# Kernel tuning notes

Measured on AMD Instinct MI355X. Metric: run time of the kernel, lower is better.

The kernel has to match this reference:

```python
import jax, jax.numpy as jnp
import numpy as np

D_MODEL = 1024
N_HEADS = 16
D_HEAD = D_MODEL // N_HEADS
LN_EPS = 1e-5


def setup_inputs() -> dict:
    key = jax.random.key(0)
    ks = jax.random.split(key, 8)
    B, T = 4, 2048
    s = 1.0 / np.sqrt(D_MODEL)
    return {
        "encoder_seq": jax.random.normal(ks[0], (B, T, D_MODEL), jnp.float32),
        "decoder_seq": jax.random.normal(ks[1], (B, T, D_MODEL), jnp.float32),
        "Wq": jax.random.normal(ks[2], (D_MODEL, D_MODEL), jnp.float32) * s,
        "bq": jnp.zeros((D_MODEL,), jnp.float32),
        "Wk": jax.random.normal(ks[3], (D_MODEL, D_MODEL), jnp.float32) * s,
        "bk": jnp.zeros((D_MODEL,), jnp.float32),
        "Wv": jax.random.normal(ks[4], (D_MODEL, D_MODEL), jnp.float32) * s,
        "bv": jnp.zeros((D_MODEL,), jnp.float32),
        "ln_gamma": jnp.ones((D_MODEL,), jnp.float32),
        "ln_beta": jnp.zeros((D_MODEL,), jnp.float32),
    }


def layer_norm(x, gamma, beta):
    mu = jnp.mean(x, axis=-1, keepdims=True)
    var = jnp.mean(jnp.square(x - mu), axis=-1, keepdims=True)
    return (x - mu) * jax.lax.rsqrt(var + LN_EPS) * gamma + beta


def reference(encoder_seq, decoder_seq, Wq, bq, Wk, bk, Wv, bv, ln_gamma, ln_beta):
    B, T_dec, _ = decoder_seq.shape
    T_enc = encoder_seq.shape[1]
    # projections (torch Linear: x @ W^T + b)
    q = (decoder_seq @ Wq.T + bq).reshape(B, T_dec, N_HEADS, D_HEAD)
    k = (encoder_seq @ Wk.T + bk).reshape(B, T_enc, N_HEADS, D_HEAD)
    v = (encoder_seq @ Wv.T + bv).reshape(B, T_enc, N_HEADS, D_HEAD)
    scale = 1.0 / np.sqrt(D_HEAD)
    # softmax-free attention: scale*(Q K^T) V == scale * Q (K^T V); avoid [T_dec,T_enc]
    kv = jnp.einsum("bthd,bthe->bhde", k, v)          # [B,H,dh,dh]
    att = jnp.einsum("bqhd,bhde->bqhe", q, kv) * scale  # [B,T_dec,H,dh]
    att = att.reshape(B, T_dec, D_MODEL)
    # dropout is identity in eval mode; residual + LayerNorm
    return layer_norm(att + decoder_seq, ln_gamma, ln_beta)
```

## Files before the change

### kernel.cpp

```cpp
#include <hip/hip_runtime.h>
#include <hip/hip_bf16.h>
#include <stdint.h>
#include <stddef.h>

typedef __attribute__((ext_vector_type(8))) __bf16 bf16x8;
typedef __attribute__((ext_vector_type(4))) float f32x4;

#define DMODEL 1024
#define HEADS  16
#define BATCH  4
#define TSEQ   2048
#define MROWS  (BATCH * TSEQ)
#define NE     (MROWS * DMODEL)
#define NW     (DMODEL * DMODEL)

#define MiB (size_t)1048576
#define QB_OFF   ((size_t)0)
#define KB_OFF   (16 * MiB)
#define VB_OFF   (32 * MiB)
#define ENC_OFF  (48 * MiB)
#define DEC_OFF  (64 * MiB)
#define KVP_OFF  (64 * MiB)
#define WB_OFF   (80 * MiB)
#define KVT_OFF  (86 * MiB)

__global__ __launch_bounds__(256)
void conv_all(const float* __restrict__ enc, const float* __restrict__ dec,
              const float* __restrict__ Wq, const float* __restrict__ Wk,
              const float* __restrict__ Wv,
              __bf16* __restrict__ encB, __bf16* __restrict__ decB,
              __bf16* __restrict__ WB)
{
    const int i = (blockIdx.x * 256 + threadIdx.x) * 8;
    const float* src;
    __bf16* dst;
    int off;
    if (i < NE)            { src = enc; dst = encB; off = i; }
    else if (i < 2 * NE)   { src = dec; dst = decB; off = i - NE; }
    else {
        const int j = i - 2 * NE;
        const int sel = j >> 20;
        off = j & (NW - 1);
        src = (sel == 0) ? Wq : (sel == 1) ? Wk : Wv;
        dst = WB + (size_t)sel * NW;
    }
    f32x4 a = *(const f32x4*)(src + off);
    f32x4 b = *(const f32x4*)(src + off + 4);
    bf16x8 o;
#pragma unroll
    for (int j = 0; j < 4; ++j) { o[j] = (__bf16)a[j]; o[j + 4] = (__bf16)b[j]; }
    *(bf16x8*)(dst + off) = o;
}

__device__ __forceinline__ int swz4(int row) { return (row & 3) ^ ((row >> 2) & 3); }

__device__ __forceinline__ bf16x8 frag32(const __bf16* reg, int rowl, int g4)
{
    const int slot = g4 ^ swz4(rowl);
    return *(const bf16x8*)(reg + rowl * 32 + slot * 8);
}

__device__ __forceinline__ void stage_half32(const __bf16* gbase, int kt,
                                             __bf16* reg, int tid)
{
    const int row = tid >> 2, slot = tid & 3;
    const __bf16* src = gbase + (size_t)row * DMODEL + kt * 32
                        + ((slot ^ swz4(row)) << 3);
    __builtin_amdgcn_global_load_lds(
        (const __attribute__((address_space(1))) void*)src,
        (__attribute__((address_space(3))) void*)(reg + tid * 8), 16, 0, 0);
}

#define VMW(N)  asm volatile("s_waitcnt vmcnt(" #N ")" ::: "memory")
#define LGKM0() asm volatile("s_waitcnt lgkmcnt(0)" ::: "memory")

__global__ __launch_bounds__(512, 4)
void qkv_gemm(const __bf16* __restrict__ decB, const __bf16* __restrict__ encB,
              const __bf16* __restrict__ WB,
              const float* __restrict__ bq, const float* __restrict__ bk,
              const float* __restrict__ bv,
              __bf16* __restrict__ Qb, __bf16* __restrict__ Kb,
              __bf16* __restrict__ Vb)
{
    __shared__ __align__(16) __bf16 ldsA[2 * 4096];
    __shared__ __align__(16) __bf16 ldsB[2 * 8192];

    const int tid  = threadIdx.x;
    const int lane = tid & 63;
    const int wv   = tid >> 6;
    const int wm   = wv >> 2;
    const int wn   = wv & 3;
    const int bh2  = wn >> 1;
    const int l4   = lane & 15;
    const int g4   = lane >> 4;

    const int bid  = blockIdx.x;
    const int slab = bid & 7;
    const int idx  = bid >> 3;
    const int r    = idx >> 3;
    const int sel  = r >> 2;
    const int bn   = r & 3;
    const int bm   = slab * 8 + (idx & 7);

    const __bf16* A    = (sel == 0) ? decB : encB;
    const __bf16* Wb   = WB + (size_t)sel * NW + (size_t)(bn * 256) * DMODEL;
    const float*  bias = (sel == 0) ? bq : (sel == 1) ? bk : bv;
    __bf16*       C    = (sel == 0) ? Qb : (sel == 1) ? Kb : Vb;

    const __bf16* Ab = A + (size_t)(bm * 128) * DMODEL;

    auto stage_tile = [&](int par, int kt) {
        stage_half32(Ab,                        kt, ldsA + par * 4096,        tid);
        stage_half32(Wb,                        kt, ldsB + par * 8192,        tid);
        stage_half32(Wb + (size_t)128 * DMODEL, kt, ldsB + par * 8192 + 4096, tid);
    };

    f32x4 acc[4][4] = {};

    stage_tile(0, 0);
    stage_tile(1, 1);
    VMW(3);
    __builtin_amdgcn_sched_barrier(0);
    __builtin_amdgcn_s_barrier();

#pragma unroll 1
    for (int t = 0; t < 32; ++t) {
        const int par = t & 1;
        const __bf16* bA = ldsA + par * 4096;
        const __bf16* bB = ldsB + par * 8192 + bh2 * 4096;

        bf16x8 af[4], bf[4];
#pragma unroll
        for (int mf = 0; mf < 4; ++mf)
            af[mf] = frag32(bA, wm * 64 + mf * 16 + l4, g4);
#pragma unroll
        for (int nf = 0; nf < 4; ++nf)
            bf[nf] = frag32(bB, (wn & 1) * 64 + nf * 16 + l4, g4);

        LGKM0();
        __builtin_amdgcn_sched_barrier(0);
        __builtin_amdgcn_s_barrier();

        if (t < 30) stage_tile(par, t + 2);

        __builtin_amdgcn_sched_barrier(0);
        __builtin_amdgcn_s_setprio(1);
#pragma unroll
        for (int mf = 0; mf < 4; ++mf)
#pragma unroll
            for (int nf = 0; nf < 4; ++nf)
                acc[mf][nf] = __builtin_amdgcn_mfma_f32_16x16x32_bf16(
                    af[mf], bf[nf], acc[mf][nf], 0, 0, 0);
        __builtin_amdgcn_s_setprio(0);

        if (t < 30)       { VMW(3); }
        else if (t == 30) { VMW(0); }
        __builtin_amdgcn_sched_barrier(0);
        __builtin_amdgcn_s_barrier();
    }

#pragma unroll
    for (int mf = 0; mf < 4; ++mf)
#pragma unroll
        for (int nf = 0; nf < 4; ++nf) {
            const int gm0 = bm * 128 + wm * 64 + mf * 16 + g4 * 4;
            const int gn  = bn * 256 + wn * 64 + nf * 16 + l4;
            const float bv2 = bias[gn];
#pragma unroll
            for (int j = 0; j < 4; ++j)
                C[(size_t)(gm0 + j) * DMODEL + gn] =
                    (__bf16)(acc[mf][nf][j] + bv2);
        }
}

__global__ __launch_bounds__(256)
void kv_mm(const __bf16* __restrict__ Kb, const __bf16* __restrict__ Vb,
           float* __restrict__ kvp)
{
    __shared__ __align__(16) float Ks[128][64];
    __shared__ __align__(16) float Vs[128][64];

    const int tid = threadIdx.x;
    const int bh  = blockIdx.x;
    const int ch  = blockIdx.y;
    const int b   = bh >> 4, h = bh & 15;
    const int w   = tid >> 6, lane = tid & 63;
    const int dg  = (lane >> 3) * 8;
    const int eg  = (lane & 7) * 8;
    const size_t base = (size_t)b * TSEQ + (size_t)ch * 512;

    f32x4 acc[8][2] = {};

    for (int ss = 0; ss < 4; ++ss) {
        __syncthreads();
#pragma unroll
        for (int i = 0; i < 4; ++i) {
            const int e = i * 2048 + tid * 8;
            const int t = e >> 6, d = e & 63;
            bf16x8 k8 = *(const bf16x8*)&Kb[(base + ss * 128 + t) * DMODEL + h * 64 + d];
            bf16x8 v8 = *(const bf16x8*)&Vb[(base + ss * 128 + t) * DMODEL + h * 64 + d];
            f32x4 kf0, kf1, vf0, vf1;
#pragma unroll
            for (int j = 0; j < 4; ++j) {
                kf0[j] = (float)k8[j]; kf1[j] = (float)k8[j + 4];
                vf0[j] = (float)v8[j]; vf1[j] = (float)v8[j + 4];
            }
            *(f32x4*)&Ks[t][d]     = kf0;
            *(f32x4*)&Ks[t][d + 4] = kf1;
            *(f32x4*)&Vs[t][d]     = vf0;
            *(f32x4*)&Vs[t][d + 4] = vf1;
        }
        __syncthreads();

#pragma unroll 4
        for (int tt = 0; tt < 32; ++tt) {
            const int t = w * 32 + tt;
            f32x4 kd0 = *(const f32x4*)&Ks[t][dg];
            f32x4 kd1 = *(const f32x4*)&Ks[t][dg + 4];
            f32x4 ve0 = *(const f32x4*)&Vs[t][eg];
            f32x4 ve1 = *(const f32x4*)&Vs[t][eg + 4];
#pragma unroll
            for (int rr = 0; rr < 8; ++rr) {
                const float kd = (rr < 4) ? kd0[rr] : kd1[rr - 4];
                acc[rr][0] += ve0 * kd;
                acc[rr][1] += ve1 * kd;
            }
        }
    }

    float* o = kvp + ((size_t)(ch * 4 + w) * 64 + bh) * 4096 + (size_t)dg * 64 + eg;
#pragma unroll
    for (int rr = 0; rr < 8; ++rr) {
        *(f32x4*)(o + rr * 64)     = acc[rr][0];
        *(f32x4*)(o + rr * 64 + 4) = acc[rr][1];
    }
}

__global__ __launch_bounds__(256)
void kv_reduce(const float* __restrict__ kvp, __bf16* __restrict__ kvT)
{
    const int idx = blockIdx.x * 256 + threadIdx.x;
    const int bh  = idx >> 12;
    const int rem = idx & 4095;
    const int d = rem >> 6, e = rem & 63;
    float s = 0.f;
#pragma unroll
    for (int c = 0; c < 16; ++c) s += kvp[((size_t)c * 64 + bh) * 4096 + rem];
    kvT[(size_t)bh * 4096 + e * 64 + d] = (__bf16)(s * 0.125f);
}

__global__ __launch_bounds__(256)
void att_ln(const __bf16* __restrict__ Q, const __bf16* __restrict__ kvT,
            const float* __restrict__ dec, const float* __restrict__ gamma,
            const float* __restrict__ beta, float* __restrict__ out)
{
    __shared__ __align__(16) __bf16 att_s[32][1032];

    const int tid  = threadIdx.x;
    const int lane = tid & 63;
    const int w    = tid >> 6;
    const int l4   = lane & 15, g4 = lane >> 4;
    const int t0   = blockIdx.x * 32;
    const int b    = t0 >> 11;

#pragma unroll
    for (int i = 0; i < 4; ++i) {
        const int h = w * 4 + i;
        f32x4 acc[2][4] = {};
#pragma unroll
        for (int kk = 0; kk < 2; ++kk) {
            bf16x8 a0 = *(const bf16x8*)&Q[(size_t)(t0 + l4) * DMODEL + h * 64 + kk * 32 + g4 * 8];
            bf16x8 a1 = *(const bf16x8*)&Q[(size_t)(t0 + 16 + l4) * DMODEL + h * 64 + kk * 32 + g4 * 8];
#pragma unroll
            for (int n = 0; n < 4; ++n) {
                bf16x8 bb = *(const bf16x8*)&kvT[(size_t)(b * 16 + h) * 4096 + (n * 16 + l4) * 64 + kk * 32 + g4 * 8];
                acc[0][n] = __builtin_amdgcn_mfma_f32_16x16x32_bf16(a0, bb, acc[0][n], 0, 0, 0);
                acc[1][n] = __builtin_amdgcn_mfma_f32_16x16x32_bf16(a1, bb, acc[1][n], 0, 0, 0);
            }
        }
#pragma unroll
        for (int m = 0; m < 2; ++m)
#pragma unroll
            for (int n = 0; n < 4; ++n)
#pragma unroll
                for (int j = 0; j < 4; ++j)
                    att_s[m * 16 + g4 * 4 + j][h * 64 + n * 16 + l4] = (__bf16)acc[m][n][j];
    }
    __syncthreads();

    const int rr = tid >> 3, seg = tid & 7;
    const size_t grow = (size_t)t0 + rr;
    float sum = 0.f, ss2 = 0.f;
#pragma unroll
    for (int i = 0; i < 16; ++i) {
        const int c0 = seg * 8 + i * 64;
        bf16x8 av = *(const bf16x8*)&att_s[rr][c0];
        f32x4 d0 = *(const f32x4*)&dec[grow * DMODEL + c0];
        f32x4 d1 = *(const f32x4*)&dec[grow * DMODEL + c0 + 4];
        bf16x8 xs;
#pragma unroll
        for (int j = 0; j < 4; ++j) {
            const float x0 = (float)av[j] + d0[j];
            const float x1 = (float)av[j + 4] + d1[j];
            sum += x0 + x1; ss2 += x0 * x0 + x1 * x1;
            xs[j] = (__bf16)x0; xs[j + 4] = (__bf16)x1;
        }
        *(bf16x8*)&att_s[rr][c0] = xs;
    }
    sum += __shfl_xor(sum, 1); ss2 += __shfl_xor(ss2, 1);
    sum += __shfl_xor(sum, 2); ss2 += __shfl_xor(ss2, 2);
    sum += __shfl_xor(sum, 4); ss2 += __shfl_xor(ss2, 4);
    const float mu   = sum * (1.f / 1024.f);
    const float var  = ss2 * (1.f / 1024.f) - mu * mu;
    const float rstd = rsqrtf(var + 1e-5f);

#pragma unroll
    for (int i = 0; i < 16; ++i) {
        const int c0 = seg * 8 + i * 64;
        bf16x8 xv = *(const bf16x8*)&att_s[rr][c0];
        f32x4 g0 = *(const f32x4*)&gamma[c0];
        f32x4 g1 = *(const f32x4*)&gamma[c0 + 4];
        f32x4 b0 = *(const f32x4*)&beta[c0];
        f32x4 b1 = *(const f32x4*)&beta[c0 + 4];
        f32x4 y0, y1;
#pragma unroll
        for (int j = 0; j < 4; ++j) {
            y0[j] = ((float)xv[j]     - mu) * rstd * g0[j] + b0[j];
            y1[j] = ((float)xv[j + 4] - mu) * rstd * g1[j] + b1[j];
        }
        *(f32x4*)&out[grow * DMODEL + c0]     = y0;
        *(f32x4*)&out[grow * DMODEL + c0 + 4] = y1;
    }
}

extern "C" void kernel_launch(void* const* d_in, const int* in_sizes, int n_in,
                              void* d_out, int out_size, void* d_ws, size_t ws_size,
                              hipStream_t stream)
{
    const float* enc   = (const float*)d_in[0];
    const float* dec   = (const float*)d_in[1];
    const float* Wq    = (const float*)d_in[2];
    const float* bq    = (const float*)d_in[3];
    const float* Wk    = (const float*)d_in[4];
    const float* bk    = (const float*)d_in[5];
    const float* Wv    = (const float*)d_in[6];
    const float* bv    = (const float*)d_in[7];
    const float* gamma = (const float*)d_in[8];
    const float* beta  = (const float*)d_in[9];

    char* ws = (char*)d_ws;
    __bf16* Qb   = (__bf16*)(ws + QB_OFF);
    __bf16* Kb   = (__bf16*)(ws + KB_OFF);
    __bf16* Vb   = (__bf16*)(ws + VB_OFF);
    __bf16* encB = (__bf16*)(ws + ENC_OFF);
    __bf16* decB = (__bf16*)(ws + DEC_OFF);
    float*  kvp  = (float*) (ws + KVP_OFF);
    __bf16* WB   = (__bf16*)(ws + WB_OFF);
    __bf16* kvT  = (__bf16*)(ws + KVT_OFF);

    conv_all<<<9728, 256, 0, stream>>>(enc, dec, Wq, Wk, Wv, encB, decB, WB);
    qkv_gemm<<<768, 512, 0, stream>>>(decB, encB, WB, bq, bk, bv, Qb, Kb, Vb);
    kv_mm<<<dim3(64, 4), 256, 0, stream>>>(Kb, Vb, kvp);
    kv_reduce<<<1024, 256, 0, stream>>>(kvp, kvT);
    att_ln<<<256, 256, 0, stream>>>(Qb, kvT, dec, gamma, beta, (float*)d_out);
}
```

Baseline: 135.1 us.

## Enlarge QKV GEMM tile to 256x256 with triple-buffered LDS and new swizzle

The QKV projection GEMM now uses 256x256 output tiles per block instead of 128x256, which halves the grid to 384 blocks and doubles the accumulator count per wave. LDS staging changes from double to triple buffering, which removes the mid-iteration barrier so each iteration needs only one barrier. It also switches to a paired-row XOR swizzle to avoid LDS bank conflicts. The aim is more reuse per loaded tile and less synchronisation, at the cost of higher register and LDS use (occupancy 1 block/CU) and fewer blocks on the 256-CU device.

```diff
diff --git a/kernel.cpp b/kernel.cpp
--- a/kernel.cpp
+++ b/kernel.cpp
@@ -52,29 +52,33 @@
     *(bf16x8*)(dst + off) = o;
 }
 
-__device__ __forceinline__ int swz4(int row) { return (row & 3) ^ ((row >> 2) & 3); }
-
-__device__ __forceinline__ bf16x8 frag32(const __bf16* reg, int rowl, int g4)
-{
-    const int slot = g4 ^ swz4(rowl);
-    return *(const bf16x8*)(reg + rowl * 32 + slot * 8);
-}
-
-__device__ __forceinline__ void stage_half32(const __bf16* gbase, int kt,
-                                             __bf16* reg, int tid)
-{
-    const int row = tid >> 2, slot = tid & 3;
-    const __bf16* src = gbase + (size_t)row * DMODEL + kt * 32
-                        + ((slot ^ swz4(row)) << 3);
-    __builtin_amdgcn_global_load_lds(
-        (const __attribute__((address_space(1))) void*)src,
-        (__attribute__((address_space(3))) void*)(reg + tid * 8), 16, 0, 0);
+__device__ __forceinline__ bf16x8 fragPP(const __bf16* buf, int row, int g4)
+{
+    const int L = row >> 1;
+    const int p = (((row & 1) << 2) | g4) ^ (L & 7);
+    return *(const bf16x8*)(buf + L * 64 + p * 8);
+}
+
+__device__ __forceinline__ void stagePP(const __bf16* gbase, int kt,
+                                        __bf16* buf, int tid)
+{
+#pragma unroll
+    for (int q = 0; q < 2; ++q) {
+        const int c = tid + q * 512;
+        const int L = c >> 3, p = c & 7;
+        const int s = p ^ (L & 7);
+        const int r = (L << 1) | (s >> 2);
+        const int kc = s & 3;
+        const __bf16* src = gbase + (size_t)r * DMODEL + kt * 32 + kc * 8;
+        __builtin_amdgcn_global_load_lds(
+            (const __attribute__((address_space(1))) void*)src,
+            (__attribute__((address_space(3))) void*)(buf + c * 8), 16, 0, 0);
+    }
 }
 
 #define VMW(N)  asm volatile("s_waitcnt vmcnt(" #N ")" ::: "memory")
-#define LGKM0() asm volatile("s_waitcnt lgkmcnt(0)" ::: "memory")
-
-__global__ __launch_bounds__(512, 4)
+
+__global__ __launch_bounds__(512, 1)
 void qkv_gemm(const __bf16* __restrict__ decB, const __bf16* __restrict__ encB,
               const __bf16* __restrict__ WB,
               const float* __restrict__ bq, const float* __restrict__ bk,
@@ -82,88 +86,84 @@
               __bf16* __restrict__ Qb, __bf16* __restrict__ Kb,
               __bf16* __restrict__ Vb)
 {
-    __shared__ __align__(16) __bf16 ldsA[2 * 4096];
-    __shared__ __align__(16) __bf16 ldsB[2 * 8192];
+    __shared__ __align__(16) __bf16 ldsA[3 * 8192];
+    __shared__ __align__(16) __bf16 ldsB[3 * 8192];
 
     const int tid  = threadIdx.x;
     const int lane = tid & 63;
     const int wv   = tid >> 6;
     const int wm   = wv >> 2;
     const int wn   = wv & 3;
-    const int bh2  = wn >> 1;
     const int l4   = lane & 15;
     const int g4   = lane >> 4;
 
     const int bid  = blockIdx.x;
     const int slab = bid & 7;
     const int idx  = bid >> 3;
-    const int r    = idx >> 3;
-    const int sel  = r >> 2;
-    const int bn   = r & 3;
-    const int bm   = slab * 8 + (idx & 7);
+    const int rr   = idx >> 2;
+    const int sel  = rr >> 2;
+    const int bn   = rr & 3;
+    const int bm   = slab * 4 + (idx & 3);
 
     const __bf16* A    = (sel == 0) ? decB : encB;
     const __bf16* Wb   = WB + (size_t)sel * NW + (size_t)(bn * 256) * DMODEL;
     const float*  bias = (sel == 0) ? bq : (sel == 1) ? bk : bv;
     __bf16*       C    = (sel == 0) ? Qb : (sel == 1) ? Kb : Vb;
 
-    const __bf16* Ab = A + (size_t)(bm * 128) * DMODEL;
-
-    auto stage_tile = [&](int par, int kt) {
-        stage_half32(Ab,                        kt, ldsA + par * 4096,        tid);
-        stage_half32(Wb,                        kt, ldsB + par * 8192,        tid);
-        stage_half32(Wb + (size_t)128 * DMODEL, kt, ldsB + par * 8192 + 4096, tid);
-    };
-
-    f32x4 acc[4][4] = {};
-
-    stage_tile(0, 0);
-    stage_tile(1, 1);
-    VMW(3);
+    const __bf16* Ab = A + (size_t)(bm * 256) * DMODEL;
+
+    f32x4 acc[8][4] = {};
+
+    stagePP(Ab, 0, ldsA, tid);          stagePP(Wb, 0, ldsB, tid);
+    stagePP(Ab, 1, ldsA + 8192, tid);   stagePP(Wb, 1, ldsB + 8192, tid);
+    VMW(4);
     __builtin_amdgcn_sched_barrier(0);
     __builtin_amdgcn_s_barrier();
-
+    __builtin_amdgcn_sched_barrier(0);
+
+    int rd = 0;
 #pragma unroll 1
     for (int t = 0; t < 32; ++t) {
-        const int par = t & 1;
-        const __bf16* bA = ldsA + par * 4096;
-        const __bf16* bB = ldsB + par * 8192 + bh2 * 4096;
-
-        bf16x8 af[4], bf[4];
-#pragma unroll
-        for (int mf = 0; mf < 4; ++mf)
-            af[mf] = frag32(bA, wm * 64 + mf * 16 + l4, g4);
+        const __bf16* bA = ldsA + rd * 8192;
+        const __bf16* bB = ldsB + rd * 8192;
+
+        bf16x8 af[8], bf[4];
+#pragma unroll
+        for (int mf = 0; mf < 8; ++mf)
+            af[mf] = fragPP(bA, wm * 128 + mf * 16 + l4, g4);
 #pragma unroll
         for (int nf = 0; nf < 4; ++nf)
-            bf[nf] = frag32(bB, (wn & 1) * 64 + nf * 16 + l4, g4);
-
-        LGKM0();
-        __builtin_amdgcn_sched_barrier(0);
-        __builtin_amdgcn_s_barrier();
-
-        if (t < 30) stage_tile(par, t + 2);
-
-        __builtin_amdgcn_sched_barrier(0);
+            bf[nf] = fragPP(bB, wn * 64 + nf * 16 + l4, g4);
+
+        const int st = (rd == 0) ? 2 : rd - 1;
+        if (t <= 29) {
+            stagePP(Ab, t + 2, ldsA + st * 8192, tid);
+            stagePP(Wb, t + 2, ldsB + st * 8192, tid);
+        }
+
         __builtin_amdgcn_s_setprio(1);
 #pragma unroll
-        for (int mf = 0; mf < 4; ++mf)
+        for (int mf = 0; mf < 8; ++mf)
 #pragma unroll
             for (int nf = 0; nf < 4; ++nf)
                 acc[mf][nf] = __builtin_amdgcn_mfma_f32_16x16x32_bf16(
                     af[mf], bf[nf], acc[mf][nf], 0, 0, 0);
         __builtin_amdgcn_s_setprio(0);
 
-        if (t < 30)       { VMW(3); }
+        if (t <= 29)      { VMW(4); }
         else if (t == 30) { VMW(0); }
         __builtin_amdgcn_sched_barrier(0);
         __builtin_amdgcn_s_barrier();
-    }
-
-#pragma unroll
-    for (int mf = 0; mf < 4; ++mf)
+        __builtin_amdgcn_sched_barrier(0);
+
+        rd = (rd == 2) ? 0 : rd + 1;
+    }
+
+#pragma unroll
+    for (int mf = 0; mf < 8; ++mf)
 #pragma unroll
         for (int nf = 0; nf < 4; ++nf) {
-            const int gm0 = bm * 128 + wm * 64 + mf * 16 + g4 * 4;
+            const int gm0 = bm * 256 + wm * 128 + mf * 16 + g4 * 4;
             const int gn  = bn * 256 + wn * 64 + nf * 16 + l4;
             const float bv2 = bias[gn];
 #pragma unroll
@@ -359,7 +359,7 @@
     __bf16* kvT  = (__bf16*)(ws + KVT_OFF);
 
     conv_all<<<9728, 256, 0, stream>>>(enc, dec, Wq, Wk, Wv, encB, decB, WB);
-    qkv_gemm<<<768, 512, 0, stream>>>(decB, encB, WB, bq, bk, bv, Qb, Kb, Vb);
+    qkv_gemm<<<384, 512, 0, stream>>>(decB, encB, WB, bq, bk, bv, Qb, Kb, Vb);
     kv_mm<<<dim3(64, 4), 256, 0, stream>>>(Kb, Vb, kvp);
     kv_reduce<<<1024, 256, 0, stream>>>(kvp, kvT);
     att_ln<<<256, 256, 0, stream>>>(Qb, kvT, dec, gamma, beta, (float*)d_out);
```

Measured after the change: 132.5 us. About the same (-1.9%).
